# Kernel optimization log

Measured on AMD Instinct MI355X. Metric: run time of the kernel, lower is better.

The kernel has to match this reference:

```python
import jax, jax.numpy as jnp
import numpy as np

HID = 1024
NTOK = 16
BIAS_SCALE = 1.5
EPS = 1e-5


def layer_norm(x, g, b):
    mu = jnp.mean(x, axis=-1, keepdims=True)
    var = jnp.mean(jnp.square(x - mu), axis=-1, keepdims=True)
    return (x - mu) * jax.lax.rsqrt(var + EPS) * g + b


def setup_inputs() -> dict:
    key = jax.random.key(0)
    ks = jax.random.split(key, 16)
    B, T = 8, 4096
    Dt, Ds, Dp = 512, 512, 64
    Din = Dt + Ds + Dp

    def lin(k, fan_in, fan_out):
        bound = 1.0 / np.sqrt(fan_in)
        k1, k2 = jax.random.split(k)
        W = jax.random.uniform(k1, (fan_in, fan_out), jnp.float32, -bound, bound)
        b = jax.random.uniform(k2, (fan_out,), jnp.float32, -bound, bound)
        return W, b

    W_in, b_in = lin(ks[0], Din, HID)
    W_m1, b_m1 = lin(ks[1], HID, HID)
    W_m2, b_m2 = lin(ks[2], HID, HID)
    W_o1, b_o1 = lin(ks[3], HID, HID // 2)
    W_o2, b_o2 = lin(ks[4], HID // 2, 1)
    return {
        "trace_features": jax.random.normal(ks[5], (B, T, Dt), jnp.float32),
        "semantic_features": jax.random.normal(ks[6], (B, T, Ds), jnp.float32),
        "prior_features": jax.random.normal(ks[7], (B, T, Dp), jnp.float32),
        "W_in": W_in, "b_in": b_in,
        "ln_in_g": jnp.ones((HID,), jnp.float32), "ln_in_b": jnp.zeros((HID,), jnp.float32),
        "W_m1": W_m1, "b_m1": b_m1, "W_m2": W_m2, "b_m2": b_m2,
        "W_o1": W_o1, "b_o1": b_o1, "W_o2": W_o2, "b_o2": b_o2,
        "token_queries": jax.random.normal(ks[8], (NTOK, HID), jnp.float32) * 0.02,
        "ln_out_g": jnp.ones((HID,), jnp.float32), "ln_out_b": jnp.zeros((HID,), jnp.float32),
    }


def reference(trace_features, semantic_features, prior_features,
              W_in, b_in, ln_in_g, ln_in_b,
              W_m1, b_m1, W_m2, b_m2,
              W_o1, b_o1, W_o2, b_o2,
              token_queries, ln_out_g, ln_out_b):
    # fuse inputs: [B, T, Dt+Ds+Dp]
    fused = jnp.concatenate([trace_features, semantic_features, prior_features], axis=-1)
    h = fused @ W_in + b_in  # [B, T, H]
    mlp = jax.nn.gelu(h @ W_m1 + b_m1, approximate=False) @ W_m2 + b_m2
    seq_hidden = layer_norm(h + mlp, ln_in_g, ln_in_b)

    # objectness head -> [B, T]
    obj_logits = (jax.nn.gelu(seq_hidden @ W_o1 + b_o1, approximate=False) @ W_o2 + b_o2)[..., 0]
    objectness = jax.nn.sigmoid(obj_logits)

    # learned-query cross attention with objectness bias
    scale = float(HID) ** -0.5
    attn_logits = jnp.einsum('nh,bth->bnt', token_queries, seq_hidden) * scale
    attn_logits = attn_logits + BIAS_SCALE * objectness[:, None, :]
    attn = jax.nn.softmax(attn_logits, axis=-1)  # [B, N, T]
    token_values = jnp.einsum('bnt,bth->bnh', attn, seq_hidden)
    state_tokens = layer_norm(token_queries[None] + token_values, ln_out_g, ln_out_b)
    return state_tokens, attn, objectness
```

## Files before the change

kernel.cpp:

```cpp
#include <hip/hip_runtime.h>
#include <hip/hip_bf16.h>
#include <math.h>

typedef __bf16 bf16;
typedef __bf16 bf16x8 __attribute__((ext_vector_type(8)));
typedef __bf16 bf16x4 __attribute__((ext_vector_type(4)));
typedef float f32x4 __attribute__((ext_vector_type(4)));

#define KM 32768
#define DIN 1088

__device__ __forceinline__ void gload16(const void* g, void* l) {
  __builtin_amdgcn_global_load_lds((const __attribute__((address_space(1))) void*)g,
                                   (__attribute__((address_space(3))) void*)l, 16, 0, 0);
}

__device__ __forceinline__ float gelu_exact(float x) {
  return 0.5f * x * (1.0f + erff(x * 0.70710678118654752f));
}

__global__ void fuse_kernel(const float* __restrict__ tr, const float* __restrict__ se,
                            const float* __restrict__ pr, bf16* __restrict__ Xb) {
  int g = blockIdx.x * 256 + threadIdx.x;
  if (g >= KM * 272) return;
  int m = g / 272;
  int k0 = (g - m * 272) * 4;
  float4 v;
  if (k0 < 512)       v = *reinterpret_cast<const float4*>(tr + (size_t)m * 512 + k0);
  else if (k0 < 1024) v = *reinterpret_cast<const float4*>(se + (size_t)m * 512 + (k0 - 512));
  else                v = *reinterpret_cast<const float4*>(pr + (size_t)m * 64 + (k0 - 1024));
  union { bf16 h[4]; ushort4 u; } p;
  p.h[0] = (bf16)v.x; p.h[1] = (bf16)v.y; p.h[2] = (bf16)v.z; p.h[3] = (bf16)v.w;
  *reinterpret_cast<ushort4*>(Xb + (size_t)m * 1088 + k0) = p.u;
}

__global__ void transpose_kernel(const float* __restrict__ W, bf16* __restrict__ Wt,
                                 int K, int N) {
  __shared__ float t[32][33];
  int k0 = blockIdx.x * 32, n0 = blockIdx.y * 32;
  int tx = threadIdx.x & 31, ty = threadIdx.x >> 5;
  #pragma unroll
  for (int j = 0; j < 32; j += 8) t[ty + j][tx] = W[(size_t)(k0 + ty + j) * N + n0 + tx];
  __syncthreads();
  #pragma unroll
  for (int j = 0; j < 32; j += 8)
    Wt[(size_t)(n0 + ty + j) * K + k0 + tx] = (bf16)t[tx][ty + j];
}

template<int ACT, bool RES>
__global__ void gemm_kernel(const bf16* __restrict__ A, const bf16* __restrict__ Bt,
                            const float* __restrict__ bias, const bf16* __restrict__ res,
                            bf16* __restrict__ C, int N, int K, int nbn) {
  __shared__ __align__(16) bf16 lds[2][128 * 64];
  int nwg = gridDim.x;
  int bid0 = blockIdx.x;
  int bid = (nwg & 7) ? bid0 : ((bid0 & 7) * (nwg >> 3) + (bid0 >> 3));
  int bn = bid % nbn, bm = bid / nbn;
  int tid = threadIdx.x;
  int w = tid >> 6, L = tid & 63;
  int wm = w >> 1, wn = w & 1;
  int srow = L >> 3;
  int scol = 8 * ((L & 7) ^ srow);
  const bf16* Ab = A + (size_t)(bm * 128) * K;
  const bf16* Bb = Bt + (size_t)(bn * 128) * K;
  f32x4 acc[4][4] = {};
  int nkt = K >> 6;
  for (int kt = 0; kt < nkt; ++kt) {
    int k0 = kt << 6;
    #pragma unroll
    for (int i = 0; i < 4; ++i) {
      int row = w * 32 + i * 8;
      gload16(Ab + (size_t)(row + srow) * K + k0 + scol, &lds[0][row * 64]);
      gload16(Bb + (size_t)(row + srow) * K + k0 + scol, &lds[1][row * 64]);
    }
    __syncthreads();
    #pragma unroll
    for (int kk = 0; kk < 2; ++kk) {
      bf16x8 af[4], bfr[4];
      int cb = kk * 64 + ((L >> 4) * 16);
      #pragma unroll
      for (int m = 0; m < 4; ++m) {
        int r = wm * 64 + m * 16 + (L & 15);
        int addr = r * 128 + (cb ^ ((r & 7) << 4));
        af[m] = *reinterpret_cast<const bf16x8*>(
            reinterpret_cast<const char*>(&lds[0][0]) + addr);
      }
      #pragma unroll
      for (int n = 0; n < 4; ++n) {
        int r = wn * 64 + n * 16 + (L & 15);
        int addr = r * 128 + (cb ^ ((r & 7) << 4));
        bfr[n] = *reinterpret_cast<const bf16x8*>(
            reinterpret_cast<const char*>(&lds[1][0]) + addr);
      }
      #pragma unroll
      for (int m = 0; m < 4; ++m)
        #pragma unroll
        for (int n = 0; n < 4; ++n)
          acc[m][n] = __builtin_amdgcn_mfma_f32_16x16x32_bf16(af[m], bfr[n], acc[m][n], 0, 0, 0);
    }
    __syncthreads();
  }
  int cn0 = bn * 128 + wn * 64;
  float bv[4];
  #pragma unroll
  for (int n = 0; n < 4; ++n) bv[n] = bias[cn0 + n * 16 + (L & 15)];
  #pragma unroll
  for (int m = 0; m < 4; ++m) {
    int grow0 = bm * 128 + wm * 64 + m * 16 + ((L >> 4) << 2);
    #pragma unroll
    for (int r = 0; r < 4; ++r) {
      size_t ro = (size_t)(grow0 + r) * N;
      #pragma unroll
      for (int n = 0; n < 4; ++n) {
        float v = acc[m][n][r] + bv[n];
        if (ACT == 1) v = gelu_exact(v);
        int col = cn0 + n * 16 + (L & 15);
        if (RES) v += (float)res[ro + col];
        C[ro + col] = (bf16)v;
      }
    }
  }
}

__global__ void ln_inplace_kernel(bf16* __restrict__ X, const float* __restrict__ g,
                                  const float* __restrict__ b) {
  __shared__ float sb[4];
  size_t row = blockIdx.x;
  bf16* xr = X + row * 1024;
  int tid = threadIdx.x;
  bf16x4 xv = *reinterpret_cast<const bf16x4*>(xr + tid * 4);
  float x[4];
  #pragma unroll
  for (int i = 0; i < 4; ++i) x[i] = (float)xv[i];
  float s = x[0] + x[1] + x[2] + x[3];
  #pragma unroll
  for (int off = 32; off > 0; off >>= 1) s += __shfl_xor(s, off);
  if ((tid & 63) == 0) sb[tid >> 6] = s;
  __syncthreads();
  float mu = (sb[0] + sb[1] + sb[2] + sb[3]) * (1.0f / 1024.0f);
  __syncthreads();
  float d[4], sq = 0.f;
  #pragma unroll
  for (int i = 0; i < 4; ++i) { d[i] = x[i] - mu; sq += d[i] * d[i]; }
  #pragma unroll
  for (int off = 32; off > 0; off >>= 1) sq += __shfl_xor(sq, off);
  if ((tid & 63) == 0) sb[tid >> 6] = sq;
  __syncthreads();
  float var = (sb[0] + sb[1] + sb[2] + sb[3]) * (1.0f / 1024.0f);
  float rs = rsqrtf(var + 1e-5f);
  bf16x4 ov;
  #pragma unroll
  for (int i = 0; i < 4; ++i) ov[i] = (bf16)(d[i] * rs * g[tid * 4 + i] + b[tid * 4 + i]);
  *reinterpret_cast<bf16x4*>(xr + tid * 4) = ov;
}

__global__ void obj_kernel(const bf16* __restrict__ o1, const float* __restrict__ W2,
                           const float* __restrict__ b2, float* __restrict__ obj,
                           float* __restrict__ out_obj) {
  __shared__ float w[512];
  int tid = threadIdx.x;
  w[tid] = W2[tid]; w[tid + 256] = W2[tid + 256];
  __syncthreads();
  int wv = tid >> 6, L = tid & 63;
  size_t m = (size_t)blockIdx.x * 4 + wv;
  bf16x8 v = *reinterpret_cast<const bf16x8*>(o1 + m * 512 + L * 8);
  float s = 0.f;
  #pragma unroll
  for (int j = 0; j < 8; ++j) s += (float)v[j] * w[L * 8 + j];
  #pragma unroll
  for (int off = 32; off > 0; off >>= 1) s += __shfl_xor(s, off);
  if (L == 0) {
    float o = 1.0f / (1.0f + expf(-(s + b2[0])));
    obj[m] = o; out_obj[m] = o;
  }
}

__global__ void attn_logits_mfma(const bf16* __restrict__ seq, const float* __restrict__ tq,
                                 const float* __restrict__ obj, float* __restrict__ logits) {
  __shared__ bf16 tqs[16][1032];
  int tid = threadIdx.x;
  for (int i = tid; i < 4096; i += 256) {
    int idx = i * 4;
    int n = idx >> 10, k = idx & 1023;
    float4 v = *reinterpret_cast<const float4*>(tq + idx);
    bf16x4 p; p[0] = (bf16)v.x; p[1] = (bf16)v.y; p[2] = (bf16)v.z; p[3] = (bf16)v.w;
    *reinterpret_cast<bf16x4*>(&tqs[n][k]) = p;
  }
  __syncthreads();
  int w = tid >> 6, L = tid & 63;
  int row0 = blockIdx.x * 128 + w * 32;
  const bf16* A0 = seq + (size_t)(row0 + (L & 15)) * 1024 + ((L >> 4) * 8);
  const bf16* Bq = &tqs[L & 15][(L >> 4) * 8];
  f32x4 acc0 = {}, acc1 = {};
  #pragma unroll 4
  for (int kt = 0; kt < 32; ++kt) {
    int k0 = kt * 32;
    bf16x8 bq = *reinterpret_cast<const bf16x8*>(Bq + k0);
    bf16x8 a0 = *reinterpret_cast<const bf16x8*>(A0 + k0);
    bf16x8 a1 = *reinterpret_cast<const bf16x8*>(A0 + 16 * 1024 + k0);
    acc0 = __builtin_amdgcn_mfma_f32_16x16x32_bf16(a0, bq, acc0, 0, 0, 0);
    acc1 = __builtin_amdgcn_mfma_f32_16x16x32_bf16(a1, bq, acc1, 0, 0, 0);
  }
  int b = row0 >> 12;
  int n = L & 15;
  float* outn = logits + ((size_t)(b * 16) + n) * 4096;
  #pragma unroll
  for (int mf = 0; mf < 2; ++mf) {
    int mrow = row0 + mf * 16 + ((L >> 4) << 2);
    #pragma unroll
    for (int r = 0; r < 4; ++r) {
      int m = mrow + r;
      float v = (mf == 0 ? acc0[r] : acc1[r]) * 0.03125f + 1.5f * obj[m];
      outn[m & 4095] = v;
    }
  }
}

__global__ void softmax_kernel(const float* __restrict__ logits, float* __restrict__ attn) {
  __shared__ float sb[4];
  size_t row = blockIdx.x;
  const float* lr = logits + row * 4096;
  float* orow = attn + row * 4096;
  int tid = threadIdx.x;
  float x[16];
  #pragma unroll
  for (int i = 0; i < 4; ++i) {
    float4 v = *reinterpret_cast<const float4*>(lr + tid * 16 + i * 4);
    x[i * 4 + 0] = v.x; x[i * 4 + 1] = v.y; x[i * 4 + 2] = v.z; x[i * 4 + 3] = v.w;
  }
  float mx = -1e30f;
  #pragma unroll
  for (int j = 0; j < 16; ++j) mx = fmaxf(mx, x[j]);
  #pragma unroll
  for (int off = 32; off > 0; off >>= 1) mx = fmaxf(mx, __shfl_xor(mx, off));
  if ((tid & 63) == 0) sb[tid >> 6] = mx;
  __syncthreads();
  mx = fmaxf(fmaxf(sb[0], sb[1]), fmaxf(sb[2], sb[3]));
  __syncthreads();
  float s = 0.f;
  #pragma unroll
  for (int j = 0; j < 16; ++j) { x[j] = expf(x[j] - mx); s += x[j]; }
  #pragma unroll
  for (int off = 32; off > 0; off >>= 1) s += __shfl_xor(s, off);
  if ((tid & 63) == 0) sb[tid >> 6] = s;
  __syncthreads();
  float inv = 1.0f / (sb[0] + sb[1] + sb[2] + sb[3]);
  #pragma unroll
  for (int i = 0; i < 4; ++i) {
    float4 v = make_float4(x[i * 4] * inv, x[i * 4 + 1] * inv, x[i * 4 + 2] * inv, x[i * 4 + 3] * inv);
    *reinterpret_cast<float4*>(orow + tid * 16 + i * 4) = v;
  }
}

__global__ void token_values_kernel(const float* __restrict__ attn, const bf16* __restrict__ seq,
                                    float* __restrict__ tvp) {
  int bid = blockIdx.x;
  int split = bid & 3;
  int hc = (bid >> 2) & 15;
  int b = bid >> 6;
  __shared__ float al[16][256];
  int h = hc * 64 + (threadIdx.x & 63);
  int grp = threadIdx.x >> 6;
  float acc[4] = {0.f, 0.f, 0.f, 0.f};
  for (int c = 0; c < 4; ++c) {
    int t0 = split * 1024 + c * 256;
    __syncthreads();
    for (int i = threadIdx.x; i < 4096; i += 256)
      al[i >> 8][i & 255] = attn[((size_t)b * 16 + (i >> 8)) * 4096 + t0 + (i & 255)];
    __syncthreads();
    for (int tt = 0; tt < 256; ++tt) {
      float s = (float)seq[((size_t)b * 4096 + t0 + tt) * 1024 + h];
      #pragma unroll
      for (int i = 0; i < 4; ++i) acc[i] += al[grp * 4 + i][tt] * s;
    }
  }
  #pragma unroll
  for (int i = 0; i < 4; ++i)
    tvp[(size_t)split * 131072 + ((size_t)b * 16 + grp * 4 + i) * 1024 + h] = acc[i];
}

__global__ void final_ln_kernel(const float* __restrict__ tq, const float* __restrict__ tvp,
                                const float* __restrict__ g, const float* __restrict__ bb,
                                float* __restrict__ out0) {
  __shared__ float sb[4];
  int row = blockIdx.x;
  int n = row & 15;
  int tid = threadIdx.x;
  float x[4];
  #pragma unroll
  for (int i = 0; i < 4; ++i) {
    int h = tid * 4 + i;
    float v = tq[n * 1024 + h];
    #pragma unroll
    for (int p = 0; p < 4; ++p) v += tvp[(size_t)p * 131072 + (size_t)row * 1024 + h];
    x[i] = v;
  }
  float s = x[0] + x[1] + x[2] + x[3];
  #pragma unroll
  for (int off = 32; off > 0; off >>= 1) s += __shfl_xor(s, off);
  if ((tid & 63) == 0) sb[tid >> 6] = s;
  __syncthreads();
  float mu = (sb[0] + sb[1] + sb[2] + sb[3]) * (1.0f / 1024.0f);
  __syncthreads();
  float d[4], sq = 0.f;
  #pragma unroll
  for (int i = 0; i < 4; ++i) { d[i] = x[i] - mu; sq += d[i] * d[i]; }
  #pragma unroll
  for (int off = 32; off > 0; off >>= 1) sq += __shfl_xor(sq, off);
  if ((tid & 63) == 0) sb[tid >> 6] = sq;
  __syncthreads();
  float var = (sb[0] + sb[1] + sb[2] + sb[3]) * (1.0f / 1024.0f);
  float rs = rsqrtf(var + 1e-5f);
  #pragma unroll
  for (int i = 0; i < 4; ++i) {
    int h = tid * 4 + i;
    out0[(size_t)row * 1024 + h] = d[i] * rs * g[h] + bb[h];
  }
}

extern "C" void kernel_launch(void* const* d_in, const int* in_sizes, int n_in,
                              void* d_out, int out_size, void* d_ws, size_t ws_size,
                              hipStream_t stream) {
  const float* tr      = (const float*)d_in[0];
  const float* se      = (const float*)d_in[1];
  const float* pr      = (const float*)d_in[2];
  const float* W_in    = (const float*)d_in[3];
  const float* b_in    = (const float*)d_in[4];
  const float* ln_in_g = (const float*)d_in[5];
  const float* ln_in_b = (const float*)d_in[6];
  const float* W_m1    = (const float*)d_in[7];
  const float* b_m1    = (const float*)d_in[8];
  const float* W_m2    = (const float*)d_in[9];
  const float* b_m2    = (const float*)d_in[10];
  const float* W_o1    = (const float*)d_in[11];
  const float* b_o1    = (const float*)d_in[12];
  const float* W_o2    = (const float*)d_in[13];
  const float* b_o2    = (const float*)d_in[14];
  const float* tq      = (const float*)d_in[15];
  const float* ln_out_g= (const float*)d_in[16];
  const float* ln_out_b= (const float*)d_in[17];

  float* out       = (float*)d_out;
  float* out_state = out;
  float* out_attn  = out + 131072;
  float* out_obj   = out + 131072 + 524288;

  char* ws = (char*)d_ws;
  size_t off = 0;
  auto alloc = [&](size_t bytes) {
    char* p = ws + off;
    off += (bytes + 255) & ~(size_t)255;
    return p;
  };
  bf16*  Xb   = (bf16*)alloc(71303168);
  bf16*  t1   = Xb;
  bf16*  hb   = (bf16*)alloc(67108864);
  bf16*  o1   = hb;
  bf16*  sq   = (bf16*)alloc(67108864);
  bf16*  WbIn = (bf16*)alloc(2228224);
  bf16*  WbM1 = (bf16*)alloc(2097152);
  bf16*  WbM2 = (bf16*)alloc(2097152);
  bf16*  WbO1 = (bf16*)alloc(1048576);
  float* objw = (float*)alloc(131072 * 4);
  float* logw = (float*)alloc(2097152);
  float* tvp  = (float*)alloc(2097152);

  fuse_kernel<<<(KM * 272 + 255) / 256, 256, 0, stream>>>(tr, se, pr, Xb);
  transpose_kernel<<<dim3(34, 32), 256, 0, stream>>>(W_in, WbIn, 1088, 1024);
  transpose_kernel<<<dim3(32, 32), 256, 0, stream>>>(W_m1, WbM1, 1024, 1024);
  transpose_kernel<<<dim3(32, 32), 256, 0, stream>>>(W_m2, WbM2, 1024, 1024);
  transpose_kernel<<<dim3(32, 16), 256, 0, stream>>>(W_o1, WbO1, 1024, 512);

  gemm_kernel<0, false><<<256 * 8, 256, 0, stream>>>(Xb, WbIn, b_in, nullptr, hb, 1024, 1088, 8);
  gemm_kernel<1, false><<<256 * 8, 256, 0, stream>>>(hb, WbM1, b_m1, nullptr, t1, 1024, 1024, 8);
  gemm_kernel<0, true ><<<256 * 8, 256, 0, stream>>>(t1, WbM2, b_m2, hb, sq, 1024, 1024, 8);
  ln_inplace_kernel<<<32768, 256, 0, stream>>>(sq, ln_in_g, ln_in_b);
  gemm_kernel<1, false><<<256 * 4, 256, 0, stream>>>(sq, WbO1, b_o1, nullptr, o1, 512, 1024, 4);
  obj_kernel<<<8192, 256, 0, stream>>>(o1, W_o2, b_o2, objw, out_obj);
  attn_logits_mfma<<<256, 256, 0, stream>>>(sq, tq, objw, logw);
  softmax_kernel<<<128, 256, 0, stream>>>(logw, out_attn);
  token_values_kernel<<<512, 256, 0, stream>>>(out_attn, sq, tvp);
  final_ln_kernel<<<128, 256, 0, stream>>>(tq, tvp, ln_out_g, ln_out_b, out_state);
}
```

Measured before the change: 438.3 us.

## Fuse input concat/convert into first GEMM and load A fragments directly from global

Removes the separate concat+bf16 conversion kernel by having the first GEMM read the three fp32 input tensors directly and convert in registers. All GEMMs now load A fragments straight from global memory into registers instead of staging them in LDS, keeping only B in shared memory. This saves a full write/read of the fused input buffer and halves LDS use. In exchange it loses A-tile sharing across waves, issues strided uncoalesced global loads in the inner loop, and doubles A bytes for the first GEMM.

Result: slower. 813.9 us (+85.7%).

```diff
diff --git a/kernel.cpp b/kernel.cpp
--- a/kernel.cpp
+++ b/kernel.cpp
@@ -8,7 +8,6 @@
 typedef float f32x4 __attribute__((ext_vector_type(4)));
 
 #define KM 32768
-#define DIN 1088
 
 __device__ __forceinline__ void gload16(const void* g, void* l) {
   __builtin_amdgcn_global_load_lds((const __attribute__((address_space(1))) void*)g,
@@ -17,21 +16,6 @@
 
 __device__ __forceinline__ float gelu_exact(float x) {
   return 0.5f * x * (1.0f + erff(x * 0.70710678118654752f));
-}
-
-__global__ void fuse_kernel(const float* __restrict__ tr, const float* __restrict__ se,
-                            const float* __restrict__ pr, bf16* __restrict__ Xb) {
-  int g = blockIdx.x * 256 + threadIdx.x;
-  if (g >= KM * 272) return;
-  int m = g / 272;
-  int k0 = (g - m * 272) * 4;
-  float4 v;
-  if (k0 < 512)       v = *reinterpret_cast<const float4*>(tr + (size_t)m * 512 + k0);
-  else if (k0 < 1024) v = *reinterpret_cast<const float4*>(se + (size_t)m * 512 + (k0 - 512));
-  else                v = *reinterpret_cast<const float4*>(pr + (size_t)m * 64 + (k0 - 1024));
-  union { bf16 h[4]; ushort4 u; } p;
-  p.h[0] = (bf16)v.x; p.h[1] = (bf16)v.y; p.h[2] = (bf16)v.z; p.h[3] = (bf16)v.w;
-  *reinterpret_cast<ushort4*>(Xb + (size_t)m * 1088 + k0) = p.u;
 }
 
 __global__ void transpose_kernel(const float* __restrict__ W, bf16* __restrict__ Wt,
@@ -47,11 +31,14 @@
     Wt[(size_t)(n0 + ty + j) * K + k0 + tx] = (bf16)t[tx][ty + j];
 }
 
-template<int ACT, bool RES>
-__global__ void gemm_kernel(const bf16* __restrict__ A, const bf16* __restrict__ Bt,
+template<int ACT, bool RES, int ASRC>
+__global__ void gemm_kernel(const bf16* __restrict__ A,
+                            const float* __restrict__ Af0, const float* __restrict__ Af1,
+                            const float* __restrict__ Af2,
+                            const bf16* __restrict__ Bt,
                             const float* __restrict__ bias, const bf16* __restrict__ res,
                             bf16* __restrict__ C, int N, int K, int nbn) {
-  __shared__ __align__(16) bf16 lds[2][128 * 64];
+  __shared__ __align__(16) bf16 lds[128 * 64];
   int nwg = gridDim.x;
   int bid0 = blockIdx.x;
   int bid = (nwg & 7) ? bid0 : ((bid0 & 7) * (nwg >> 3) + (bid0 >> 3));
@@ -61,42 +48,61 @@
   int wm = w >> 1, wn = w & 1;
   int srow = L >> 3;
   int scol = 8 * ((L & 7) ^ srow);
-  const bf16* Ab = A + (size_t)(bm * 128) * K;
   const bf16* Bb = Bt + (size_t)(bn * 128) * K;
   f32x4 acc[4][4] = {};
-  int nkt = K >> 6;
+  int nkt = (K + 63) >> 6;
+  int arow = bm * 128 + wm * 64 + (L & 15);
+  int aoff = (L >> 4) * 8;
   for (int kt = 0; kt < nkt; ++kt) {
     int k0 = kt << 6;
     #pragma unroll
     for (int i = 0; i < 4; ++i) {
       int row = w * 32 + i * 8;
-      gload16(Ab + (size_t)(row + srow) * K + k0 + scol, &lds[0][row * 64]);
-      gload16(Bb + (size_t)(row + srow) * K + k0 + scol, &lds[1][row * 64]);
+      gload16(Bb + (size_t)(row + srow) * K + k0 + scol, &lds[row * 64]);
+    }
+    bf16x8 af[4][2];
+    if (ASRC == 0) {
+      #pragma unroll
+      for (int m = 0; m < 4; ++m)
+        #pragma unroll
+        for (int kk = 0; kk < 2; ++kk)
+          af[m][kk] = *reinterpret_cast<const bf16x8*>(
+              A + (size_t)(arow + m * 16) * K + k0 + kk * 32 + aoff);
+    } else {
+      const float* fsrc; int fstride, fk;
+      if (kt < 8)       { fsrc = Af0; fstride = 512; fk = k0; }
+      else if (kt < 16) { fsrc = Af1; fstride = 512; fk = k0 - 512; }
+      else              { fsrc = Af2; fstride = 64;  fk = 0; }
+      #pragma unroll
+      for (int m = 0; m < 4; ++m)
+        #pragma unroll
+        for (int kk = 0; kk < 2; ++kk) {
+          const float4* p = reinterpret_cast<const float4*>(
+              fsrc + (size_t)(arow + m * 16) * fstride + fk + kk * 32 + aoff);
+          float4 v0 = p[0], v1 = p[1];
+          bf16x8 t;
+          t[0] = (bf16)v0.x; t[1] = (bf16)v0.y; t[2] = (bf16)v0.z; t[3] = (bf16)v0.w;
+          t[4] = (bf16)v1.x; t[5] = (bf16)v1.y; t[6] = (bf16)v1.z; t[7] = (bf16)v1.w;
+          af[m][kk] = t;
+        }
     }
     __syncthreads();
     #pragma unroll
     for (int kk = 0; kk < 2; ++kk) {
-      bf16x8 af[4], bfr[4];
+      bf16x8 bfr[4];
       int cb = kk * 64 + ((L >> 4) * 16);
-      #pragma unroll
-      for (int m = 0; m < 4; ++m) {
-        int r = wm * 64 + m * 16 + (L & 15);
-        int addr = r * 128 + (cb ^ ((r & 7) << 4));
-        af[m] = *reinterpret_cast<const bf16x8*>(
-            reinterpret_cast<const char*>(&lds[0][0]) + addr);
-      }
       #pragma unroll
       for (int n = 0; n < 4; ++n) {
         int r = wn * 64 + n * 16 + (L & 15);
         int addr = r * 128 + (cb ^ ((r & 7) << 4));
         bfr[n] = *reinterpret_cast<const bf16x8*>(
-            reinterpret_cast<const char*>(&lds[1][0]) + addr);
+            reinterpret_cast<const char*>(&lds[0]) + addr);
       }
       #pragma unroll
       for (int m = 0; m < 4; ++m)
         #pragma unroll
         for (int n = 0; n < 4; ++n)
-          acc[m][n] = __builtin_amdgcn_mfma_f32_16x16x32_bf16(af[m], bfr[n], acc[m][n], 0, 0, 0);
+          acc[m][n] = __builtin_amdgcn_mfma_f32_16x16x32_bf16(af[m][kk], bfr[n], acc[m][n], 0, 0, 0);
     }
     __syncthreads();
   }
@@ -352,8 +358,7 @@
     off += (bytes + 255) & ~(size_t)255;
     return p;
   };
-  bf16*  Xb   = (bf16*)alloc(71303168);
-  bf16*  t1   = Xb;
+  bf16*  t1   = (bf16*)alloc(67108864);
   bf16*  hb   = (bf16*)alloc(67108864);
   bf16*  o1   = hb;
   bf16*  sq   = (bf16*)alloc(67108864);
@@ -365,17 +370,20 @@
   float* logw = (float*)alloc(2097152);
   float* tvp  = (float*)alloc(2097152);
 
-  fuse_kernel<<<(KM * 272 + 255) / 256, 256, 0, stream>>>(tr, se, pr, Xb);
   transpose_kernel<<<dim3(34, 32), 256, 0, stream>>>(W_in, WbIn, 1088, 1024);
   transpose_kernel<<<dim3(32, 32), 256, 0, stream>>>(W_m1, WbM1, 1024, 1024);
   transpose_kernel<<<dim3(32, 32), 256, 0, stream>>>(W_m2, WbM2, 1024, 1024);
   transpose_kernel<<<dim3(32, 16), 256, 0, stream>>>(W_o1, WbO1, 1024, 512);
 
-  gemm_kernel<0, false><<<256 * 8, 256, 0, stream>>>(Xb, WbIn, b_in, nullptr, hb, 1024, 1088, 8);
-  gemm_kernel<1, false><<<256 * 8, 256, 0, stream>>>(hb, WbM1, b_m1, nullptr, t1, 1024, 1024, 8);
-  gemm_kernel<0, true ><<<256 * 8, 256, 0, stream>>>(t1, WbM2, b_m2, hb, sq, 1024, 1024, 8);
+  gemm_kernel<0, false, 1><<<256 * 8, 256, 0, stream>>>(
+      nullptr, tr, se, pr, WbIn, b_in, nullptr, hb, 1024, 1088, 8);
+  gemm_kernel<1, false, 0><<<256 * 8, 256, 0, stream>>>(
+      hb, nullptr, nullptr, nullptr, WbM1, b_m1, nullptr, t1, 1024, 1024, 8);
+  gemm_kernel<0, true, 0><<<256 * 8, 256, 0, stream>>>(
+      t1, nullptr, nullptr, nullptr, WbM2, b_m2, hb, sq, 1024, 1024, 8);
   ln_inplace_kernel<<<32768, 256, 0, stream>>>(sq, ln_in_g, ln_in_b);
-  gemm_kernel<1, false><<<256 * 4, 256, 0, stream>>>(sq, WbO1, b_o1, nullptr, o1, 512, 1024, 4);
+  gemm_kernel<1, false, 0><<<256 * 4, 256, 0, stream>>>(
+      sq, nullptr, nullptr, nullptr, WbO1, b_o1, nullptr, o1, 512, 1024, 4);
   obj_kernel<<<8192, 256, 0, stream>>>(o1, W_o2, b_o2, objw, out_obj);
   attn_logits_mfma<<<256, 256, 0, stream>>>(sq, tq, objw, logw);
   softmax_kernel<<<128, 256, 0, stream>>>(logw, out_attn);
```
